# Kernel optimization log

Measured on AMD Instinct MI355X. Metric: run time of the kernel, lower is better.

Reference implementation:

```python
import jax, jax.numpy as jnp
import numpy as np
from jax import lax

B, TZ, TT = 16, 2048, 512
D, DFF, L, V, HEADS = 256, 1024, 6, 512, 4
CH, HID, K, FLOWS, G = 256, 256, 5, 4, 256
PAD_ID = 0
NEG = -1e9
SCALE = 0.02


def setup_inputs():
    key = jax.random.key(0)
    ks = jax.random.split(key, 20)
    n = lambda i, shape, s=SCALE: jax.random.normal(ks[i], shape, jnp.float32) * s
    return {
        'z': jax.random.normal(ks[0], (B, TZ, CH), jnp.float32),
        'text': jax.random.randint(ks[1], (B, TT), 1, V),  # low=1 so no pad tokens
        'cond': jax.random.normal(ks[2], (B, G), jnp.float32),
        'embed': n(3, (V, D), 1.0),
        'wq': n(4, (L, D, D)), 'wk': n(5, (L, D, D)), 'wv': n(6, (L, D, D)), 'wo': n(7, (L, D, D)),
        'bq': jnp.zeros((L, D)), 'bk': jnp.zeros((L, D)), 'bv': jnp.zeros((L, D)), 'bo': jnp.zeros((L, D)),
        'ln1_g': jnp.ones((L, D)), 'ln1_b': jnp.zeros((L, D)),
        'ln2_g': jnp.ones((L, D)), 'ln2_b': jnp.zeros((L, D)),
        'w1': n(8, (L, D, DFF)), 'b1': jnp.zeros((L, DFF)),
        'w2': n(9, (L, DFF, D)), 'b2': jnp.zeros((L, D)),
        'mu_w': n(10, (D, D)), 'mu_b': jnp.zeros((D,)),
        'lv_w': n(11, (D, D)), 'lv_b': jnp.zeros((D,)),
        'flow_in': n(12, (FLOWS, CH // 2, HID)), 'flow_in_b': jnp.zeros((FLOWS, HID)),
        'flow_cond': n(13, (FLOWS, G, HID)),
        'flow_conv': n(14, (FLOWS, K, HID, HID)), 'flow_conv_b': jnp.zeros((FLOWS, HID)),
        'flow_out': n(15, (FLOWS, HID, CH // 2)), 'flow_out_b': jnp.zeros((FLOWS, CH // 2)),
    }


def _pos_encoding(length, d):
    pos = np.arange(length)[:, None].astype(np.float32)
    i = np.arange(d)[None, :]
    angle = pos / np.power(10000.0, (2 * (i // 2)) / d)
    pe = np.where(i % 2 == 0, np.sin(angle), np.cos(angle))
    return jnp.asarray(pe, jnp.float32)


def _ln(x, g, b):
    m = jnp.mean(x, -1, keepdims=True)
    v = jnp.var(x, -1, keepdims=True)
    return g * (x - m) * lax.rsqrt(v + 1e-6) + b


def _mha(x, wq, wk, wv, wo, bq, bk, bv, bo, bias):
    Bq, T, _ = x.shape
    dh = D // HEADS
    heads = lambda y: y.reshape(Bq, T, HEADS, dh).transpose(0, 2, 1, 3)
    q, k, v = heads(x @ wq + bq), heads(x @ wk + bk), heads(x @ wv + bv)
    scores = jnp.einsum('bhqd,bhkd->bhqk', q, k) / jnp.sqrt(jnp.float32(dh)) + bias
    attn = jax.nn.softmax(scores, axis=-1)
    out = jnp.einsum('bhqk,bhkd->bhqd', attn, v).transpose(0, 2, 1, 3).reshape(Bq, T, D)
    return out @ wo + bo


def _mas_path(logp, text_mask):
    # Viterbi monotonic alignment: each latent frame t maps to text index j(t),
    # j nondecreasing with steps in {0, 1}, start at 0, end at last valid token.
    Bq, Tz, Tt = logp.shape
    Q0 = jnp.where(jnp.arange(Tt) == 0, logp[:, 0, :], NEG)

    def fwd(Q, lt):
        Qs = jnp.concatenate([jnp.full((Bq, 1), NEG, Q.dtype), Q[:, :-1]], axis=1)
        return lt + jnp.maximum(Q, Qs), Qs > Q  # choice True => came from j-1

    _, choices = lax.scan(fwd, Q0, jnp.swapaxes(logp, 0, 1)[1:])  # [Tz-1,B,Tt]
    j_last = jnp.sum(text_mask, axis=1).astype(jnp.int32) - 1

    def bwd(j, ch):
        c = jnp.take_along_axis(ch, j[:, None], axis=1)[:, 0]
        jp = j - c.astype(jnp.int32)
        return jp, jp

    _, path_rev = lax.scan(bwd, j_last, choices[::-1])
    path = jnp.concatenate([path_rev[::-1], j_last[None]], axis=0)  # [Tz,B]
    return jnp.swapaxes(path, 0, 1)


def _forward(z, text, cond, embed, wq, wk, wv, wo, bq, bk, bv, bo, ln1_g, ln1_b, ln2_g, ln2_b,
             w1, b1, w2, b2, mu_w, mu_b, lv_w, lv_b,
             flow_in, flow_in_b, flow_cond, flow_conv, flow_conv_b, flow_out, flow_out_b):
    text_mask = text != PAD_ID  # [B,TT]
    bias = jnp.where(text_mask[:, None, None, :], 0.0, NEG)
    # text encoder: scaled embedding + sinusoidal PE + post-LN transformer blocks
    h = embed[text] * jnp.sqrt(jnp.float32(D)) + _pos_encoding(TT, D)[None]
    for l in range(L):
        h = _ln(h + _mha(h, wq[l], wk[l], wv[l], wo[l], bq[l], bk[l], bv[l], bo[l], bias), ln1_g[l], ln1_b[l])
        ffn = jax.nn.relu(h @ w1[l] + b1[l]) @ w2[l] + b2[l]
        h = _ln(h + ffn, ln2_g[l], ln2_b[l])
    mu = h @ mu_w + mu_b
    logvar = h @ lv_w + lv_b
    # residual coupling flows (mean-only, conditioned on global vector)
    zc = z
    for f in range(FLOWS):
        x0, x1 = jnp.split(zc, 2, axis=-1)
        hh = x0 @ flow_in[f] + flow_in_b[f] + (cond @ flow_cond[f])[:, None, :]
        hh = jnp.tanh(lax.conv_general_dilated(hh, flow_conv[f], (1,), 'SAME', rhs_dilation=(1,),
                                               dimension_numbers=('NWC', 'WIO', 'NWC')) + flow_conv_b[f])
        m = hh @ flow_out[f] + flow_out_b[f]
        zc = jnp.concatenate([x1 + m, x0], axis=-1)  # coupling + flip
    # gaussian log-likelihood between latent frames and text distributions
    spr = jnp.exp(-logvar)  # [B,TT,D]
    nc1 = jnp.sum(-0.5 * jnp.log(2.0 * jnp.pi) - 0.5 * logvar, axis=-1)  # [B,TT]
    nc2 = jnp.einsum('btd,bjd->btj', -0.5 * zc * zc, spr)
    nc3 = jnp.einsum('btd,bjd->btj', zc, mu * spr)
    nc4 = jnp.sum(-0.5 * mu * mu * spr, axis=-1)  # [B,TT]
    logp = nc1[:, None, :] + nc2 + nc3 + nc4[:, None, :]  # [B,TZ,TT]
    logp = jnp.where(text_mask[:, None, :], logp, NEG)
    path = _mas_path(logp, text_mask)  # [B,TZ] int32
    ctx = mu[jnp.arange(B)[:, None], path]  # expand text mu along latent time
    return ctx, h


def reference(z, text, cond, embed, wq, wk, wv, wo, bq, bk, bv, bo, ln1_g, ln1_b, ln2_g, ln2_b,
              w1, b1, w2, b2, mu_w, mu_b, lv_w, lv_b,
              flow_in, flow_in_b, flow_cond, flow_conv, flow_conv_b, flow_out, flow_out_b):
    return _forward(z, text, cond, embed, wq, wk, wv, wo, bq, bk, bv, bo, ln1_g, ln1_b, ln2_g, ln2_b,
                    w1, b1, w2, b2, mu_w, mu_b, lv_w, lv_b,
                    flow_in, flow_in_b, flow_cond, flow_conv, flow_conv_b, flow_out, flow_out_b)
```

## Files before the change

kernel.cpp:

```cpp
#include <hip/hip_runtime.h>

#define BB 16
#define TZ_ 2048
#define TT_ 512
#define D_ 256
#define DFF_ 1024
#define L_ 6
#define HEADS_ 4
#define DH_ 64
#define CH_ 256
#define HID_ 256
#define KCV 5
#define FLOWS_ 4
#define G_ 256
#define NEGF (-1000000000.0f)
#define LOG2PI 1.8378770664093453f

typedef unsigned short u16;
typedef __attribute__((ext_vector_type(8))) short short8v;
typedef __attribute__((ext_vector_type(4))) float f32x4;

__device__ __forceinline__ float wsum(float v){
#pragma unroll
  for (int o = 32; o; o >>= 1) v += __shfl_xor(v, o);
  return v;
}
__device__ __forceinline__ u16 f2bf(float x){
  unsigned u = __float_as_uint(x);
  return (u16)((u + 0x7FFFu + ((u >> 16) & 1u)) >> 16);
}
__device__ __forceinline__ float bf2f(u16 h){
  return __uint_as_float(((unsigned)h) << 16);
}
__device__ __forceinline__ unsigned pk2f(float a, float b){
  return __builtin_amdgcn_perm(__float_as_uint(b), __float_as_uint(a), 0x07060302u);
}
__device__ __forceinline__ float trnc(float f){
  return __uint_as_float(__float_as_uint(f) & 0xFFFF0000u);
}
__device__ __forceinline__ void cvt8t(float4 x, float4 y, uint4 &hi, uint4 &lo){
  hi.x = pk2f(x.x, x.y); hi.y = pk2f(x.z, x.w);
  hi.z = pk2f(y.x, y.y); hi.w = pk2f(y.z, y.w);
  float r0 = x.x - trnc(x.x), r1 = x.y - trnc(x.y), r2 = x.z - trnc(x.z), r3 = x.w - trnc(x.w);
  float r4 = y.x - trnc(y.x), r5 = y.y - trnc(y.y), r6 = y.z - trnc(y.z), r7 = y.w - trnc(y.w);
  lo.x = pk2f(r0, r1); lo.y = pk2f(r2, r3); lo.z = pk2f(r4, r5); lo.w = pk2f(r6, r7);
}
__device__ __forceinline__ unsigned rneh(float f){
  unsigned v = __float_as_uint(f);
  return (v + 0x7FFFu + ((v >> 16) & 1u)) & 0xFFFF0000u;
}
__device__ __forceinline__ void cvt8r(float4 x, float4 y, uint4 &hi, uint4 &lo){
  unsigned h0=rneh(x.x), h1=rneh(x.y), h2=rneh(x.z), h3=rneh(x.w);
  unsigned h4=rneh(y.x), h5=rneh(y.y), h6=rneh(y.z), h7=rneh(y.w);
  hi.x = h1 | (h0>>16); hi.y = h3 | (h2>>16); hi.z = h5 | (h4>>16); hi.w = h7 | (h6>>16);
  float r0 = x.x - __uint_as_float(h0), r1 = x.y - __uint_as_float(h1);
  float r2 = x.z - __uint_as_float(h2), r3 = x.w - __uint_as_float(h3);
  float r4 = y.x - __uint_as_float(h4), r5 = y.y - __uint_as_float(h5);
  float r6 = y.z - __uint_as_float(h6), r7 = y.w - __uint_as_float(h7);
  lo.x = pk2f(r0, r1); lo.y = pk2f(r2, r3); lo.z = pk2f(r4, r5); lo.w = pk2f(r6, r7);
}

__global__ void k_pe(float* __restrict__ pe){
  int t = blockIdx.x, d = threadIdx.x;
  double e = (double)(2*(d>>1)) / (double)D_;
  double ang = (double)t * pow(10000.0, -e);
  pe[t*D_ + d] = (float)(((d&1)==0) ? sin(ang) : cos(ang));
}
__global__ void k_embed(const int* __restrict__ text, const float* __restrict__ emb,
                        const float* __restrict__ pe, float* __restrict__ h){
  int row = blockIdx.x, d = threadIdx.x;
  h[(size_t)row*D_ + d] = emb[(size_t)text[row]*D_ + d]*16.0f + pe[(row%TT_)*D_ + d];
}

__global__ __launch_bounds__(256) void k_wt(
  const float* __restrict__ wq, const float* __restrict__ wk,
  const float* __restrict__ wv, const float* __restrict__ wo,
  const float* __restrict__ mu_w, const float* __restrict__ lv_w,
  const float* __restrict__ w1, const float* __restrict__ w2,
  float* __restrict__ QKVT, float* __restrict__ OT, float* __restrict__ MULVT,
  float* __restrict__ W1T, float* __restrict__ W2T)
{
  __shared__ float td[64][65];
  const int s = blockIdx.y, tile = blockIdx.x, t = threadIdx.x;
  const float* inb; float* outb; int istride, ostride;
  if (s < 24){
    int l = s>>2, wsel = s&3;
    const float* w = (wsel==0?wq:wsel==1?wk:wsel==2?wv:wo);
    inb = w + (size_t)l*65536; istride = 256;
    if (wsel < 3) outb = QKVT + (size_t)l*196608 + wsel*65536;
    else          outb = OT   + (size_t)l*65536;
    ostride = 256;
  } else if (s < 26){
    inb = (s==24 ? mu_w : lv_w); istride = 256;
    outb = MULVT + (size_t)(s-24)*65536; ostride = 256;
  } else if (s < 50){
    int idx = s-26, l = idx>>2, b2 = idx&3;
    inb = w1 + (size_t)l*262144 + b2*256; istride = 1024;
    outb = W1T + (size_t)l*262144 + (size_t)b2*65536; ostride = 256;
  } else {
    int idx = s-50, l = idx>>2, b2 = idx&3;
    inb = w2 + (size_t)l*262144 + (size_t)b2*65536; istride = 256;
    outb = W2T + (size_t)l*262144 + b2*256; ostride = 1024;
  }
  const int kt = (tile>>2)*64, nt = (tile&3)*64;
  const int r = t>>2, cq = (t&3)*16;
#pragma unroll
  for (int c=0;c<16;c+=4){
    float4 v = *(const float4*)(inb + (size_t)(kt + r)*istride + nt + cq + c);
    td[r][cq+c+0]=v.x; td[r][cq+c+1]=v.y; td[r][cq+c+2]=v.z; td[r][cq+c+3]=v.w;
  }
  __syncthreads();
#pragma unroll
  for (int c=0;c<16;c+=4){
    float4 v = make_float4(td[cq+c+0][r], td[cq+c+1][r], td[cq+c+2][r], td[cq+c+3][r]);
    *(float4*)(outb + (size_t)(nt + r)*ostride + kt + cq + c) = v;
  }
}

__global__ __launch_bounds__(256) void k_vt(const float* __restrict__ QKV, float* __restrict__ VT){
  __shared__ float td[64][65];
  const int b = blockIdx.z, dt = blockIdx.x, jt = blockIdx.y, t = threadIdx.x;
  const float* inb = QKV + (size_t)b*512*768 + 512;
  float* outb = VT + (size_t)b*131072;
  const int r = t>>2, cq = (t&3)*16;
#pragma unroll
  for (int c=0;c<16;c+=4){
    float4 v = *(const float4*)(inb + (size_t)(jt*64 + r)*768 + dt*64 + cq + c);
    td[r][cq+c+0]=v.x; td[r][cq+c+1]=v.y; td[r][cq+c+2]=v.z; td[r][cq+c+3]=v.w;
  }
  __syncthreads();
#pragma unroll
  for (int c=0;c<16;c+=4){
    float4 v = make_float4(td[cq+c+0][r], td[cq+c+1][r], td[cq+c+2][r], td[cq+c+3][r]);
    *(float4*)(outb + (size_t)(dt*64 + r)*512 + jt*64 + cq + c) = v;
  }
}

__global__ void k_bcat(const float* __restrict__ bq, const float* __restrict__ bk,
                       const float* __restrict__ bv, const float* __restrict__ mu_b,
                       const float* __restrict__ lv_b,
                       float* __restrict__ BQKV, float* __restrict__ MULVB){
  int i = blockIdx.x*256 + threadIdx.x;
  if (i < 4608){
    int l = i/768, c = i%768;
    float v = c<256 ? bq[l*256+c] : (c<512 ? bk[l*256+c-256] : bv[l*256+c-512]);
    BQKV[i] = v;
  } else if (i < 5120){
    int c = i-4608;
    MULVB[c] = c<256 ? mu_b[c] : lv_b[c-256];
  }
}

template<int WN, int EPI, int AM, int BMD>
__global__ __launch_bounds__(256,2) void k_mg(
  const void* __restrict__ Ap, const void* __restrict__ ApL, int lda, int azhi, int azlo,
  const void* __restrict__ Bp, const void* __restrict__ BpL, int ldb, int bzhi, int bzlo,
  const float* __restrict__ bias, const int* __restrict__ text,
  const float* __restrict__ nc1v, const float* __restrict__ nc4v,
  float* __restrict__ C, int ldc, int czhi, int czlo, int K)
{
  constexpr int BN = WN*32;
  __shared__ u16 AH[4096], AL[4096];
  __shared__ u16 BH[BN*32], BL[BN*32];
  char* AHB=(char*)AH; char* ALB=(char*)AL; char* BHB=(char*)BH; char* BLB=(char*)BL;
  const int t = threadIdx.x, z = blockIdx.z;
  const int m0 = blockIdx.y*128, n0 = blockIdx.x*BN;
  const size_t aoff = (size_t)(z>>2)*azhi + (size_t)(z&3)*azlo;
  const size_t boff = (size_t)(z>>2)*bzhi + (size_t)(z&3)*bzlo;
  const size_t coff = (size_t)(z>>2)*czhi + (size_t)(z&3)*czlo;
  const int w = t>>6, l = t&63;
  const int wr = (w>>1)*64, wc = (w&1)*(WN*16);
  const int lr = l&15, lg = l>>4;
  const int srow = t>>1, sseg = t&1;
  const int q  = (srow>>1)&3;
  const int wo0 = srow*64 + ((((sseg<<1)|0)^q)<<4);
  const int wo1 = srow*64 + ((((sseg<<1)|1)^q)<<4);
  const bool bact = (WN==4) || (t < 128);
  const int qa = ((wr+lr)>>1)&3, qb2 = ((wc+lr)>>1)&3;
  const int raBase = (wr+lr)*64 + ((lg^qa)<<4);
  const int rbBase = (wc+lr)*64 + ((lg^qb2)<<4);

  const float* Af = nullptr; const u16* AfH = nullptr; const u16* AfL = nullptr;
  if constexpr (AM==0 || AM==2){ Af = (const float*)Ap + aoff; }
  else { AfH = (const u16*)Ap + aoff; AfL = (const u16*)ApL + aoff; }
  const float* Bf = nullptr; const u16* BfH = nullptr; const u16* BfL = nullptr;
  if constexpr (BMD==0){ Bf = (const float*)Bp + boff; }
  else { BfH = (const u16*)Bp + boff; BfL = (const u16*)BpL + boff; }

  f32x4 acc[4][WN];
#pragma unroll
  for (int i=0;i<4;i++)
#pragma unroll
    for (int j=0;j<WN;j++) acc[i][j] = (f32x4){0.f,0.f,0.f,0.f};

  for (int k0 = 0; k0 < K; k0 += 32){
    uint4 ahi0, ahi1, alo0, alo1;
    if constexpr (AM==0){
      const float* p = Af + (size_t)(m0+srow)*lda + k0 + sseg*16;
      float4 a0=*(const float4*)p, a1=*(const float4*)(p+4);
      float4 a2=*(const float4*)(p+8), a3=*(const float4*)(p+12);
      cvt8t(a0,a1,ahi0,alo0); cvt8t(a2,a3,ahi1,alo1);
    } else if constexpr (AM==1){
      const u16* ph = AfH + (size_t)(m0+srow)*lda + k0 + sseg*16;
      const u16* pl = AfL + (size_t)(m0+srow)*lda + k0 + sseg*16;
      ahi0 = *(const uint4*)ph; ahi1 = *(const uint4*)(ph+8);
      alo0 = *(const uint4*)pl; alo1 = *(const uint4*)(pl+8);
    } else {
      int kg = k0 + sseg*16;
      const float* p = Af + (size_t)(m0+srow)*lda + (kg < 256 ? kg : kg - 256);
      float4 a0=*(const float4*)p, a1=*(const float4*)(p+4);
      float4 a2=*(const float4*)(p+8), a3=*(const float4*)(p+12);
      if (kg >= 256){
        a0.x=-0.5f*a0.x*a0.x; a0.y=-0.5f*a0.y*a0.y; a0.z=-0.5f*a0.z*a0.z; a0.w=-0.5f*a0.w*a0.w;
        a1.x=-0.5f*a1.x*a1.x; a1.y=-0.5f*a1.y*a1.y; a1.z=-0.5f*a1.z*a1.z; a1.w=-0.5f*a1.w*a1.w;
        a2.x=-0.5f*a2.x*a2.x; a2.y=-0.5f*a2.y*a2.y; a2.z=-0.5f*a2.z*a2.z; a2.w=-0.5f*a2.w*a2.w;
        a3.x=-0.5f*a3.x*a3.x; a3.y=-0.5f*a3.y*a3.y; a3.z=-0.5f*a3.z*a3.z; a3.w=-0.5f*a3.w*a3.w;
      }
      cvt8r(a0,a1,ahi0,alo0); cvt8r(a2,a3,ahi1,alo1);
    }
    uint4 bhi0, bhi1, blo0, blo1;
    if (bact){
      if constexpr (BMD==0){
        const float* p = Bf + (size_t)(n0+srow)*ldb + k0 + sseg*16;
        float4 b0=*(const float4*)p, b1=*(const float4*)(p+4);
        float4 b2=*(const float4*)(p+8), b3=*(const float4*)(p+12);
        cvt8t(b0,b1,bhi0,blo0); cvt8t(b2,b3,bhi1,blo1);
      } else {
        const u16* ph = BfH + (size_t)(n0+srow)*ldb + k0 + sseg*16;
        const u16* pl = BfL + (size_t)(n0+srow)*ldb + k0 + sseg*16;
        bhi0 = *(const uint4*)ph; bhi1 = *(const uint4*)(ph+8);
        blo0 = *(const uint4*)pl; blo1 = *(const uint4*)(pl+8);
      }
    }
    __syncthreads();
    *(uint4*)(AHB + wo0) = ahi0;  *(uint4*)(AHB + wo1) = ahi1;
    *(uint4*)(ALB + wo0) = alo0;  *(uint4*)(ALB + wo1) = alo1;
    if (bact){
      *(uint4*)(BHB + wo0) = bhi0;  *(uint4*)(BHB + wo1) = bhi1;
      *(uint4*)(BLB + wo0) = blo0;  *(uint4*)(BLB + wo1) = blo1;
    }
    __syncthreads();
    short8v fah[4], fal[4], fbh[WN], fbl[WN];
#pragma unroll
    for (int i=0;i<4;i++){
      fah[i] = *(short8v*)(AHB + raBase + i*1024);
      fal[i] = *(short8v*)(ALB + raBase + i*1024);
    }
#pragma unroll
    for (int j=0;j<WN;j++){
      fbh[j] = *(short8v*)(BHB + rbBase + j*1024);
      fbl[j] = *(short8v*)(BLB + rbBase + j*1024);
    }
#pragma unroll
    for (int i=0;i<4;i++)
#pragma unroll
      for (int j=0;j<WN;j++){
        acc[i][j] = __builtin_amdgcn_mfma_f32_16x16x32_bf16(fah[i], fbh[j], acc[i][j], 0,0,0);
        acc[i][j] = __builtin_amdgcn_mfma_f32_16x16x32_bf16(fal[i], fbh[j], acc[i][j], 0,0,0);
        acc[i][j] = __builtin_amdgcn_mfma_f32_16x16x32_bf16(fah[i], fbl[j], acc[i][j], 0,0,0);
      }
  }

#pragma unroll
  for (int i=0;i<4;i++){
    int mm0 = m0 + wr + i*16 + (lg<<2);
#pragma unroll
    for (int j=0;j<WN;j++){
      int nn = n0 + wc + j*16 + lr;
      float bs = 0.f; float ncb = 0.f; bool msk = true;
      if (EPI==0 || EPI==1) bs = bias ? bias[nn] : 0.f;
      if (EPI==2) msk = (text[(z>>2)*TT_ + nn] != 0);
      if (EPI==3){ ncb = nc1v[z*TT_+nn] + nc4v[z*TT_+nn]; msk = (text[z*TT_+nn] != 0); }
      f32x4 v = acc[i][j];
#pragma unroll
      for (int r=0;r<4;r++){
        int m = mm0 + r;
        float x;
        if (EPI==0)      x = v[r] + bs;
        else if (EPI==1) x = fmaxf(v[r] + bs, 0.f);
        else if (EPI==2) x = v[r]*0.125f + (msk ? 0.f : NEGF);
        else             x = msk ? (v[r] + ncb) : NEGF;
        C[coff + (size_t)m*ldc + nn] = x;
      }
    }
  }
}

__global__ __launch_bounds__(64) void k_softmax(float* __restrict__ S){
  size_t row = blockIdx.x;
  float* p = S + row*TT_;
  int ln = threadIdx.x;
  float4 a = *(float4*)(p + ln*8);
  float4 b = *(float4*)(p + ln*8 + 4);
  float x[8] = {a.x,a.y,a.z,a.w,b.x,b.y,b.z,b.w};
  float m = x[0];
#pragma unroll
  for (int i=1;i<8;i++) m = fmaxf(m, x[i]);
#pragma unroll
  for (int o2=32;o2;o2>>=1) m = fmaxf(m, __shfl_xor(m, o2));
  float s = 0.f;
#pragma unroll
  for (int i=0;i<8;i++){ x[i] = expf(x[i]-m); s += x[i]; }
  s = wsum(s);
  float inv = 1.0f/s;
  *(float4*)(p + ln*8)     = make_float4(x[0]*inv, x[1]*inv, x[2]*inv, x[3]*inv);
  *(float4*)(p + ln*8 + 4) = make_float4(x[4]*inv, x[5]*inv, x[6]*inv, x[7]*inv);
}

__global__ __launch_bounds__(256) void k_lnres(const float* __restrict__ y,
  const float* __restrict__ g, const float* __restrict__ bb, float* __restrict__ h){
  size_t row = blockIdx.x; int d = threadIdx.x;
  float v = h[row*D_ + d] + y[row*D_ + d];
  float s = wsum(v), s2 = wsum(v*v);
  __shared__ float r1[4], r2[4];
  int w = d >> 6;
  if ((d & 63) == 0){ r1[w] = s; r2[w] = s2; }
  __syncthreads();
  s  = r1[0]+r1[1]+r1[2]+r1[3];
  s2 = r2[0]+r2[1]+r2[2]+r2[3];
  float mean = s * (1.0f/D_);
  float var  = s2 * (1.0f/D_) - mean*mean;
  float inv  = rsqrtf(var + 1e-6f);
  h[row*D_ + d] = g[d]*(v - mean)*inv + bb[d];
}

__global__ __launch_bounds__(256) void k_prep(const float* __restrict__ mulv,
  u16* __restrict__ b2h, u16* __restrict__ b2l,
  float* __restrict__ nc1, float* __restrict__ nc4){
  size_t row = blockIdx.x; int d = threadIdx.x;
  float m = mulv[row*512 + d];
  float lv = mulv[row*512 + 256 + d];
  float sp = expf(-lv);
  float ms = m*sp;
  float s1 = wsum(lv), s2 = wsum(m*ms);
  __shared__ float r1[4], r2[4];
  int w = d >> 6;
  if ((d&63)==0){ r1[w]=s1; r2[w]=s2; }
  __syncthreads();
  if (d == 0){
    nc1[row] = -0.5f*((float)D_*LOG2PI + (r1[0]+r1[1]+r1[2]+r1[3]));
    nc4[row] = -0.5f*(r2[0]+r2[1]+r2[2]+r2[3]);
  }
  unsigned hm = rneh(ms);
  b2h[row*512 + d] = (u16)(hm>>16);
  b2l[row*512 + d] = f2bf(ms - __uint_as_float(hm));
  unsigned hs = rneh(sp);
  b2h[row*512 + 256 + d] = (u16)(hs>>16);
  b2l[row*512 + 256 + d] = f2bf(sp - __uint_as_float(hs));
}

__global__ __launch_bounds__(256) void k_condproj(const float* __restrict__ cond,
  const float* __restrict__ W, float* __restrict__ out){
  const int b = blockIdx.x, n = threadIdx.x;
  float s = 0.f;
  for (int k2=0;k2<G_;k2++) s = fmaf(cond[b*G_ + k2], W[k2*HID_ + n], s);
  out[b*HID_ + n] = s;
}

__global__ void k_wprep2(const float* __restrict__ win, const float* __restrict__ wconv,
                         const float* __restrict__ wout,
                         u16* __restrict__ WITH, u16* __restrict__ WITL,
                         u16* __restrict__ WCTH, u16* __restrict__ WCTL,
                         u16* __restrict__ WOTH, u16* __restrict__ WOTL){
  int i = blockIdx.x*256 + threadIdx.x;
  float wv2; u16 *dh, *dl; int idx;
  if (i < 32768){
    int n = i >> 7, k = i & 127;
    wv2 = win[k*256 + n]; dh = WITH; dl = WITL; idx = i;
  } else if (i < 32768 + 327680){
    int jj = i - 32768;
    int o = jj / 1280, r = jj - o*1280;
    wv2 = wconv[(size_t)r*256 + o]; dh = WCTH; dl = WCTL; idx = jj;
  } else {
    int jj = i - 360448;
    int o = jj >> 8, k = jj & 255;
    wv2 = wout[k*128 + o]; dh = WOTH; dl = WOTL; idx = jj;
  }
  u16 hh = f2bf(wv2);
  dh[idx] = hh;
  dl[idx] = f2bf(wv2 - bf2f(hh));
}

__global__ void k_x0prep2(const float* __restrict__ z, u16* __restrict__ xh, u16* __restrict__ xl){
  size_t i = ((size_t)blockIdx.x*256 + threadIdx.x) << 3;
  size_t m2 = i >> 7; int k = (int)(i & 127);
  const float* src = z + m2*256 + k;
  float4 a = *(const float4*)src; float4 b2 = *(const float4*)(src+4);
  float vv[8] = {a.x,a.y,a.z,a.w,b2.x,b2.y,b2.z,b2.w};
  short8v oh, ol;
#pragma unroll
  for (int r=0;r<8;r++){
    u16 hh = f2bf(vv[r]);
    oh[r] = (short)hh;
    ol[r] = (short)f2bf(vv[r] - bf2f(hh));
  }
  *(short8v*)(xh + i) = oh;
  *(short8v*)(xl + i) = ol;
}

__global__ void k_padzero2(u16* __restrict__ XpH, u16* __restrict__ XpL){
  int i = blockIdx.x*256 + threadIdx.x;
  u16* P = (i >> 14) ? XpL : XpH;
  int ii = i & 16383;
  int b = ii >> 10, rr = (ii >> 8) & 3, c = ii & 255;
  int row = (rr < 2) ? rr : (2048 + rr);
  P[((size_t)b*2052 + row)*256 + c] = 0;
}

template<int EPI, int SPLITOUT>
__global__ __launch_bounds__(256,2) void k_mf2(
  const u16* __restrict__ Ah, const u16* __restrict__ Al, int lda, int padA,
  const u16* __restrict__ Bh, const u16* __restrict__ Bl, int ldb,
  const float* __restrict__ bias, const float* __restrict__ cnd,
  void* __restrict__ CH, void* __restrict__ CL, int ldc, int padC, int K)
{
  __shared__ u16 AsmH[4096], AsmL[4096], BsmH[4096], BsmL[4096];
  char* AHB=(char*)AsmH; char* ALB=(char*)AsmL;
  char* BHB=(char*)BsmH; char* BLB=(char*)BsmL;
  const int t = threadIdx.x;
  const int m0 = blockIdx.y << 7, n0 = blockIdx.x << 7;
  const int w = t >> 6, l = t & 63;
  const int wr = (w >> 1) << 6, wc = (w & 1) << 6;
  const int lr = l & 15, lg = l >> 4;
  const int srow = t >> 1, sseg = t & 1;
  const int q = (srow >> 1) & 3;
  const int wo0 = srow*64 + ((((sseg<<1)|0) ^ q) << 4);
  const int wo1 = srow*64 + ((((sseg<<1)|1) ^ q) << 4);
  const int am = m0 + srow;
  const size_t aoff = (size_t)(am + padA*(am >> 11))*lda + (sseg << 4);
  const u16* AhP = Ah + aoff;
  const u16* AlP = Al + aoff;
  const size_t boff = (size_t)(n0 + srow)*ldb + (sseg << 4);
  const u16* BhP = Bh + boff;
  const u16* BlP = Bl + boff;
  const int qa = ((wr + lr) >> 1) & 3, qb = ((wc + lr) >> 1) & 3;
  const int raBase = (wr + lr)*64 + ((lg ^ qa) << 4);
  const int rbBase = (wc + lr)*64 + ((lg ^ qb) << 4);
  f32x4 acc[4][4];
#pragma unroll
  for (int i=0;i<4;i++)
#pragma unroll
    for (int j=0;j<4;j++) acc[i][j] = (f32x4){0.f,0.f,0.f,0.f};

  for (int k0 = 0; k0 < K; k0 += 32){
    float4 ah0 = *(const float4*)(AhP + k0);
    float4 ah1 = *(const float4*)(AhP + k0 + 8);
    float4 al0 = *(const float4*)(AlP + k0);
    float4 al1 = *(const float4*)(AlP + k0 + 8);
    float4 bh0 = *(const float4*)(BhP + k0);
    float4 bh1 = *(const float4*)(BhP + k0 + 8);
    float4 bl0 = *(const float4*)(BlP + k0);
    float4 bl1 = *(const float4*)(BlP + k0 + 8);
    __syncthreads();
    *(float4*)(AHB + wo0) = ah0;  *(float4*)(AHB + wo1) = ah1;
    *(float4*)(ALB + wo0) = al0;  *(float4*)(ALB + wo1) = al1;
    *(float4*)(BHB + wo0) = bh0;  *(float4*)(BHB + wo1) = bh1;
    *(float4*)(BLB + wo0) = bl0;  *(float4*)(BLB + wo1) = bl1;
    __syncthreads();
    short8v fah[4], fal[4], fbh[4], fbl[4];
#pragma unroll
    for (int i=0;i<4;i++){
      fah[i] = *(short8v*)(AHB + raBase + i*1024);
      fal[i] = *(short8v*)(ALB + raBase + i*1024);
    }
#pragma unroll
    for (int j=0;j<4;j++){
      fbh[j] = *(short8v*)(BHB + rbBase + j*1024);
      fbl[j] = *(short8v*)(BLB + rbBase + j*1024);
    }
#pragma unroll
    for (int i=0;i<4;i++)
#pragma unroll
      for (int j=0;j<4;j++){
        acc[i][j] = __builtin_amdgcn_mfma_f32_16x16x32_bf16(fah[i], fbh[j], acc[i][j], 0, 0, 0);
        acc[i][j] = __builtin_amdgcn_mfma_f32_16x16x32_bf16(fal[i], fbh[j], acc[i][j], 0, 0, 0);
        acc[i][j] = __builtin_amdgcn_mfma_f32_16x16x32_bf16(fah[i], fbl[j], acc[i][j], 0, 0, 0);
      }
  }

#pragma unroll
  for (int i=0;i<4;i++){
    int mbase = m0 + wr + i*16 + (lg << 2);
#pragma unroll
    for (int j=0;j<4;j++){
      int nn = n0 + wc + j*16 + lr;
      float bs = bias[nn];
      f32x4 v = acc[i][j];
#pragma unroll
      for (int r=0;r<4;r++){
        int m = mbase + r;
        float x = v[r] + bs;
        if (EPI == 1) x += cnd[((m >> 11) << 8) + nn];
        if (EPI == 2) x = tanhf(x);
        if (EPI == 3) x += cnd[(size_t)m*256 + 128 + nn];
        size_t ro = (size_t)(m + padC*(m >> 11))*ldc + nn;
        if (SPLITOUT){
          u16 xh = f2bf(x);
          ((u16*)CH)[ro] = xh;
          ((u16*)CL)[ro] = f2bf(x - bf2f(xh));
        } else {
          ((float*)CH)[ro] = x;
        }
      }
    }
  }
}

__global__ void k_x0copy(const float* __restrict__ src, float* __restrict__ dst){
  size_t i = ((size_t)blockIdx.x*256 + threadIdx.x) << 2;
  size_t row = i >> 7; int c = (int)(i & 127);
  *(float4*)(dst + row*256 + 128 + c) = *(const float4*)(src + row*256 + c);
}

#define MCH 8
#define NCHK (TZ_/MCH)
__device__ __forceinline__ void mas_rows(const float* __restrict__ bp, int ch, float* Q,
                                         int ln, unsigned char* __restrict__ cb){
  for (int rr = 0; rr < MCH; rr++){
    int tr = ch*MCH + rr;
    if (tr == 0){
      float q0 = bp[0];
      if (ln == 0) Q[0] = q0;
      continue;
    }
    float4 u0 = *(const float4*)(bp + rr*TT_ + ln*8);
    float4 u1 = *(const float4*)(bp + rr*TT_ + ln*8 + 4);
    float v[8] = {u0.x,u0.y,u0.z,u0.w,u1.x,u1.y,u1.z,u1.w};
    float qp = __shfl_up(Q[7], 1);
    if (ln == 0) qp = NEGF;
    unsigned bits = 0; float qs = qp;
#pragma unroll
    for (int i=0;i<8;i++){
      float old = Q[i];
      if (qs > old) bits |= (1u<<i);
      Q[i] = v[i] + fmaxf(old, qs);
      qs = old;
    }
    cb[(size_t)(tr-1)*64 + ln] = (unsigned char)bits;
  }
}

__global__ __launch_bounds__(512) void k_mas(const float* __restrict__ lp,
  const int* __restrict__ text, unsigned char* __restrict__ cho, int* __restrict__ path)
{
  const int b = blockIdx.x, t = threadIdx.x, ln = t & 63;
  const float* L = lp + (size_t)b*TZ_*TT_;
  __shared__ float buf[3][MCH*TT_];
  __shared__ __align__(16) unsigned char lch[64*64];
  const int frow = t >> 6;
  const int fcol = (t & 63) * 8;
  const size_t gsrc = (size_t)frow*TT_ + fcol;
  unsigned char* cb = cho + (size_t)b*TZ_*64;
  {
    float4 a0 = *(const float4*)(L + gsrc);
    float4 a1 = *(const float4*)(L + gsrc + 4);
    float4 c0 = *(const float4*)(L + (size_t)MCH*TT_ + gsrc);
    float4 c1 = *(const float4*)(L + (size_t)MCH*TT_ + gsrc + 4);
    *(float4*)&buf[0][(size_t)frow*TT_+fcol]   = a0;
    *(float4*)&buf[0][(size_t)frow*TT_+fcol+4] = a1;
    *(float4*)&buf[1][(size_t)frow*TT_+fcol]   = c0;
    *(float4*)&buf[1][(size_t)frow*TT_+fcol+4] = c1;
  }
  float4 pA0 = *(const float4*)(L + (size_t)2*MCH*TT_ + gsrc);
  float4 pA1 = *(const float4*)(L + (size_t)2*MCH*TT_ + gsrc + 4);
  float4 pB0 = *(const float4*)(L + (size_t)3*MCH*TT_ + gsrc);
  float4 pB1 = *(const float4*)(L + (size_t)3*MCH*TT_ + gsrc + 4);
  __syncthreads();
  float Q[8];
#pragma unroll
  for (int i=0;i<8;i++) Q[i] = NEGF;
  int cur = 0;
#define MAS_STEP(CH, P0, P1) do { \
    int wslot = cur + 2; if (wslot >= 3) wslot -= 3; \
    if ((CH) + 2 < NCHK){ \
      *(float4*)&buf[wslot][(size_t)frow*TT_+fcol]   = P0; \
      *(float4*)&buf[wslot][(size_t)frow*TT_+fcol+4] = P1; \
    } \
    if ((CH) + 4 < NCHK){ \
      P0 = *(const float4*)(L + (size_t)((CH)+4)*MCH*TT_ + gsrc); \
      P1 = *(const float4*)(L + (size_t)((CH)+4)*MCH*TT_ + gsrc + 4); \
    } \
    if (t < 64) mas_rows(&buf[cur][0], (CH), Q, ln, cb); \
    __syncthreads(); \
    cur++; if (cur >= 3) cur = 0; \
  } while(0)
  for (int ch = 0; ch < NCHK; ch += 2){
    MAS_STEP(ch,   pA0, pA1);
    MAS_STEP(ch+1, pB0, pB1);
  }
#undef MAS_STEP
  int j = 0;
  if (t < 64){
    int cnt = 0;
#pragma unroll
    for (int i=0;i<8;i++) cnt += (text[b*TT_ + ln*8 + i] != 0) ? 1 : 0;
#pragma unroll
    for (int o2=32;o2;o2>>=1) cnt += __shfl_xor(cnt, o2);
    j = cnt - 1;
  }
  if (t == 0) path[b*TZ_ + TZ_-1] = j;
  __syncthreads();
  for (int tc = TZ_-1; tc >= 1; tc -= 64){
    int ns = min(64, tc);
    if (t < 256){
      int s = t >> 2, c = (t & 3) << 4;
      if (s < ns)
        *(float4*)&lch[s*64 + c] = *(const float4*)&cb[(size_t)(tc-1-s)*64 + c];
    }
    __syncthreads();
    if (t == 0){
      for (int s=0;s<ns;s++){
        unsigned bits = lch[s*64 + (j>>3)];
        j -= (int)((bits >> (j&7)) & 1u);
        path[b*TZ_ + tc - s - 1] = j;
      }
    }
    __syncthreads();
  }
}

__global__ void k_gather(const float* __restrict__ mulv, const int* __restrict__ path,
  const float* __restrict__ h, float* __restrict__ out){
  size_t i = (size_t)blockIdx.x*256 + threadIdx.x;
  const size_t N4 = (size_t)BB*TZ_*(D_/4);
  const size_t H4 = (size_t)BB*TT_*(D_/4);
  if (i < N4){
    size_t row = i >> 6; int c = (int)(i & 63);
    int b = (int)(row >> 11);
    int pj = path[row];
    ((float4*)out)[i] = *(const float4*)(mulv + ((size_t)b*TT_ + pj)*512 + (size_t)c*4);
  } else if (i < N4 + H4){
    size_t k2 = i - N4;
    ((float4*)out)[i] = ((const float4*)h)[k2];
  }
}

extern "C" void kernel_launch(void* const* d_in, const int* in_sizes, int n_in,
                              void* d_out, int out_size, void* d_ws, size_t ws_size,
                              hipStream_t stream)
{
  (void)in_sizes; (void)n_in; (void)out_size; (void)ws_size;
  const float* z      = (const float*)d_in[0];
  const int*   text   = (const int*)  d_in[1];
  const float* cond   = (const float*)d_in[2];
  const float* emb    = (const float*)d_in[3];
  const float* wq     = (const float*)d_in[4];
  const float* wk     = (const float*)d_in[5];
  const float* wv     = (const float*)d_in[6];
  const float* wo     = (const float*)d_in[7];
  const float* bq     = (const float*)d_in[8];
  const float* bk     = (const float*)d_in[9];
  const float* bv     = (const float*)d_in[10];
  const float* bo     = (const float*)d_in[11];
  const float* ln1g   = (const float*)d_in[12];
  const float* ln1b   = (const float*)d_in[13];
  const float* ln2g   = (const float*)d_in[14];
  const float* ln2b   = (const float*)d_in[15];
  const float* w1     = (const float*)d_in[16];
  const float* b1     = (const float*)d_in[17];
  const float* w2     = (const float*)d_in[18];
  const float* b2     = (const float*)d_in[19];
  const float* mu_w   = (const float*)d_in[20];
  const float* mu_b   = (const float*)d_in[21];
  const float* lv_w   = (const float*)d_in[22];
  const float* lv_b   = (const float*)d_in[23];
  const float* f_in   = (const float*)d_in[24];
  const float* f_in_b = (const float*)d_in[25];
  const float* f_cond = (const float*)d_in[26];
  const float* f_conv = (const float*)d_in[27];
  const float* f_convb= (const float*)d_in[28];
  const float* f_out  = (const float*)d_in[29];
  const float* f_outb = (const float*)d_in[30];

  float* ws = (float*)d_ws;
  size_t o = 0;
  float* PE   = ws + o; o += (size_t)131072;
  float* H    = ws + o; o += (size_t)2097152;
  float* MULV = ws + o; o += (size_t)4194304;
  float* NC1  = ws + o; o += (size_t)8192;
  float* NC4  = ws + o; o += (size_t)8192;
  float* CONDP= ws + o; o += (size_t)4096;
  int*   PATH = (int*)(ws + o); o += (size_t)32768;
  u16*  B2H  = (u16*)(ws + o); o += (size_t)2097152;
  u16*  B2L  = (u16*)(ws + o); o += (size_t)2097152;
  float* BIGS = ws + o; o += (size_t)16777216;
  float* BUF1 = ws + o; o += (size_t)4587520;
  float* BUF2 = ws + o; o += (size_t)10485760;
  float* ZCA  = ws + o; o += (size_t)8388608;
  float* ZCB  = ws + o; o += (size_t)8388608;

  float* QKV = BUF2;
  float* Yb  = QKV + 6291456;
  float* VT  = Yb + 2097152;
  float* ATTO= QKV;
  float* QKVT = ZCA;
  float* OT   = QKVT + 1179648;
  float* W1T  = OT + 393216;
  float* W2T  = W1T + 1572864;
  float* MULVT= W2T + 1572864;
  float* BQKV = MULVT + 131072;
  float* MULVB= BQKV + 4608;
  u16*  X0H = (u16*)BUF1;
  u16*  X0L = X0H + 4194304;
  u16*  WITH = X0L + 4194304;
  u16*  WITL = WITH + 32768;
  u16*  WCTH = WITL + 32768;
  u16*  WCTL = WCTH + 327680;
  u16*  WOTH = WCTL + 327680;
  u16*  WOTL = WOTH + 32768;
  u16*  XpH = (u16*)BIGS;
  u16*  XpL = XpH + 8404992;
  u16*  H2H = (u16*)BUF2;
  u16*  H2L = H2H + 8388608;
  unsigned char* CHO = (unsigned char*)ZCA;

  k_pe   <<<dim3(TT_),    dim3(D_), 0, stream>>>(PE);
  k_embed<<<dim3(BB*TT_), dim3(D_), 0, stream>>>(text, emb, PE, H);
  k_wt   <<<dim3(16,74), 256, 0, stream>>>(wq,wk,wv,wo,mu_w,lv_w,w1,w2, QKVT,OT,MULVT,W1T,W2T);
  k_bcat <<<dim3(20), 256, 0, stream>>>(bq,bk,bv,mu_b,lv_b, BQKV, MULVB);

  for (int l=0;l<L_;l++){
    k_mg<4,0,0,0><<<dim3(6,64,1),256,0,stream>>>(
      H, nullptr, 256, 0,0,  QKVT + (size_t)l*196608, nullptr, 256, 0,0,
      BQKV + l*768, nullptr, nullptr, nullptr, QKV, 768, 0,0, 256);
    k_vt <<<dim3(4,8,16),256,0,stream>>>(QKV, VT);
    k_mg<4,2,0,0><<<dim3(4,4,64),256,0,stream>>>(
      QKV, nullptr, 768, 393216, 64,  QKV+256, nullptr, 768, 393216, 64,
      nullptr, text, nullptr, nullptr, BIGS, 512, 1048576, 262144, 64);
    k_softmax<<<dim3(BB*HEADS_*TT_),64,0,stream>>>(BIGS);
    k_mg<2,0,0,0><<<dim3(1,4,64),256,0,stream>>>(
      BIGS, nullptr, 512, 1048576, 262144,  VT, nullptr, 512, 131072, 32768,
      nullptr, nullptr, nullptr, nullptr, Yb, 256, 131072, 64, 512);
    k_mg<4,0,0,0><<<dim3(2,64,1),256,0,stream>>>(
      Yb, nullptr, 256, 0,0,  OT + (size_t)l*65536, nullptr, 256, 0,0,
      bo + l*256, nullptr, nullptr, nullptr, ATTO, 256, 0,0, 256);
    k_lnres<<<dim3(BB*TT_),256,0,stream>>>(ATTO, ln1g+l*D_, ln1b+l*D_, H);
    k_mg<4,1,0,0><<<dim3(8,64,1),256,0,stream>>>(
      H, nullptr, 256, 0,0,  W1T + (size_t)l*262144, nullptr, 256, 0,0,
      b1 + l*1024, nullptr, nullptr, nullptr, BIGS, 1024, 0,0, 256);
    k_mg<4,0,0,0><<<dim3(2,64,1),256,0,stream>>>(
      BIGS, nullptr, 1024, 0,0,  W2T + (size_t)l*262144, nullptr, 1024, 0,0,
      b2 + l*256, nullptr, nullptr, nullptr, ATTO, 256, 0,0, 1024);
    k_lnres<<<dim3(BB*TT_),256,0,stream>>>(ATTO, ln2g+l*D_, ln2b+l*D_, H);
  }

  k_mg<4,0,0,0><<<dim3(4,64,1),256,0,stream>>>(
    H, nullptr, 256, 0,0,  MULVT, nullptr, 256, 0,0,
    MULVB, nullptr, nullptr, nullptr, MULV, 512, 0,0, 256);
  k_prep<<<dim3(BB*TT_),256,0,stream>>>(MULV, B2H, B2L, NC1, NC4);

  k_padzero2<<<dim3(128),256,0,stream>>>(XpH, XpL);
  const float* zsrc = z;
  for (int f=0; f<FLOWS_; f++){
    k_condproj<<<dim3(BB),256,0,stream>>>(cond, f_cond + (size_t)f*G_*HID_, CONDP);
    k_wprep2<<<dim3(1536),256,0,stream>>>(f_in + (size_t)f*(CH_/2)*HID_,
                                          f_conv + (size_t)f*KCV*HID_*HID_,
                                          f_out + (size_t)f*HID_*(CH_/2),
                                          WITH, WITL, WCTH, WCTL, WOTH, WOTL);
    k_x0prep2<<<dim3(2048),256,0,stream>>>(zsrc, X0H, X0L);
    k_mf2<1,1><<<dim3(2,256),256,0,stream>>>(X0H, X0L, 128, 0, WITH, WITL, 128,
        f_in_b + f*HID_, CONDP, (void*)(XpH + 512), (void*)(XpL + 512), 256, 4, 128);
    k_mf2<2,1><<<dim3(2,256),256,0,stream>>>(XpH, XpL, 256, 4, WCTH, WCTL, 1280,
        f_convb + f*HID_, nullptr, (void*)H2H, (void*)H2L, 256, 0, 1280);
    float* zdst = (f & 1) ? ZCB : ZCA;
    k_mf2<3,0><<<dim3(1,256),256,0,stream>>>(H2H, H2L, 256, 0, WOTH, WOTL, 256,
        f_outb + f*(CH_/2), zsrc, (void*)zdst, nullptr, 256, 0, 256);
    k_x0copy<<<dim3(4096),256,0,stream>>>(zsrc, zdst);
    zsrc = zdst;
  }

  k_mg<4,3,2,1><<<dim3(4,16,16),256,0,stream>>>(
    zsrc, nullptr, 256, 2097152, 524288,
    B2H, B2L, 512, 1048576, 262144,
    nullptr, text, NC1, NC4, BIGS, 512, 4194304, 1048576, 512);

  k_mas<<<dim3(BB),512,0,stream>>>(BIGS, text, CHO, PATH);
  k_gather<<<dim3((BB*TZ_*D_/4 + BB*TT_*D_/4)/256),256,0,stream>>>(MULV, PATH, H, (float*)d_out);
}
```

Baseline: 2.483 ms.

## Pipeline MAS forward/backtrack, fuse flow prep kernels, widen softmax blocks

Restructures the MAS kernel. The forward DP gets a swizzled LDS layout and register-prefetched rows, and the backtrack prefetches choice bytes into a triple-buffered LDS ring with per-row lookahead instead of one serial loop per 64-step chunk. The three flow prep kernels (weight transpose/split, x0 split, cond projection) merge into one launch, and the x0 copy is folded into the output GEMM epilogue. Softmax now handles four rows per 256-thread block. This cuts launch overhead and serial latency in MAS at the cost of more register pressure and more complex indexing.

After: 2.685 ms. +8.2%, slower.

```diff
diff --git a/kernel.cpp b/kernel.cpp
--- a/kernel.cpp
+++ b/kernel.cpp
@@ -286,10 +286,10 @@
   }
 }
 
-__global__ __launch_bounds__(64) void k_softmax(float* __restrict__ S){
-  size_t row = blockIdx.x;
+__global__ __launch_bounds__(256) void k_softmax(float* __restrict__ S){
+  size_t row = (size_t)blockIdx.x*4 + (threadIdx.x >> 6);
   float* p = S + row*TT_;
-  int ln = threadIdx.x;
+  int ln = threadIdx.x & 63;
   float4 a = *(float4*)(p + ln*8);
   float4 b = *(float4*)(p + ln*8 + 4);
   float x[8] = {a.x,a.y,a.z,a.w,b.x,b.y,b.z,b.w};
@@ -349,53 +349,54 @@
   b2l[row*512 + 256 + d] = f2bf(sp - __uint_as_float(hs));
 }
 
-__global__ __launch_bounds__(256) void k_condproj(const float* __restrict__ cond,
-  const float* __restrict__ W, float* __restrict__ out){
-  const int b = blockIdx.x, n = threadIdx.x;
-  float s = 0.f;
-  for (int k2=0;k2<G_;k2++) s = fmaf(cond[b*G_ + k2], W[k2*HID_ + n], s);
-  out[b*HID_ + n] = s;
-}
-
-__global__ void k_wprep2(const float* __restrict__ win, const float* __restrict__ wconv,
-                         const float* __restrict__ wout,
-                         u16* __restrict__ WITH, u16* __restrict__ WITL,
-                         u16* __restrict__ WCTH, u16* __restrict__ WCTL,
-                         u16* __restrict__ WOTH, u16* __restrict__ WOTL){
-  int i = blockIdx.x*256 + threadIdx.x;
-  float wv2; u16 *dh, *dl; int idx;
-  if (i < 32768){
-    int n = i >> 7, k = i & 127;
-    wv2 = win[k*256 + n]; dh = WITH; dl = WITL; idx = i;
-  } else if (i < 32768 + 327680){
-    int jj = i - 32768;
-    int o = jj / 1280, r = jj - o*1280;
-    wv2 = wconv[(size_t)r*256 + o]; dh = WCTH; dl = WCTL; idx = jj;
+__global__ __launch_bounds__(256) void k_fprep(
+  const float* __restrict__ win, const float* __restrict__ wconv, const float* __restrict__ wout,
+  u16* __restrict__ WITH, u16* __restrict__ WITL,
+  u16* __restrict__ WCTH, u16* __restrict__ WCTL,
+  u16* __restrict__ WOTH, u16* __restrict__ WOTL,
+  const float* __restrict__ zsrc, u16* __restrict__ xh, u16* __restrict__ xl,
+  const float* __restrict__ cond, const float* __restrict__ fcw, float* __restrict__ condp)
+{
+  const int bid = blockIdx.x, t = threadIdx.x;
+  if (bid < 1536){
+    int i = bid*256 + t;
+    float wv2; u16 *dh, *dl; int idx;
+    if (i < 32768){
+      int n = i >> 7, k = i & 127;
+      wv2 = win[k*256 + n]; dh = WITH; dl = WITL; idx = i;
+    } else if (i < 360448){
+      int jj = i - 32768;
+      int o = jj / 1280, r = jj - o*1280;
+      wv2 = wconv[(size_t)r*256 + o]; dh = WCTH; dl = WCTL; idx = jj;
+    } else {
+      int jj = i - 360448;
+      int o = jj >> 8, k = jj & 255;
+      wv2 = wout[k*128 + o]; dh = WOTH; dl = WOTL; idx = jj;
+    }
+    u16 hh = f2bf(wv2);
+    dh[idx] = hh;
+    dl[idx] = f2bf(wv2 - bf2f(hh));
+  } else if (bid < 3584){
+    size_t i = ((size_t)(bid-1536)*256 + t) << 3;
+    size_t m2 = i >> 7; int k = (int)(i & 127);
+    const float* src = zsrc + m2*256 + k;
+    float4 a = *(const float4*)src; float4 b2 = *(const float4*)(src+4);
+    float vv[8] = {a.x,a.y,a.z,a.w,b2.x,b2.y,b2.z,b2.w};
+    short8v oh, ol;
+#pragma unroll
+    for (int r=0;r<8;r++){
+      u16 hh = f2bf(vv[r]);
+      oh[r] = (short)hh;
+      ol[r] = (short)f2bf(vv[r] - bf2f(hh));
+    }
+    *(short8v*)(xh + i) = oh;
+    *(short8v*)(xl + i) = ol;
   } else {
-    int jj = i - 360448;
-    int o = jj >> 8, k = jj & 255;
-    wv2 = wout[k*128 + o]; dh = WOTH; dl = WOTL; idx = jj;
-  }
-  u16 hh = f2bf(wv2);
-  dh[idx] = hh;
-  dl[idx] = f2bf(wv2 - bf2f(hh));
-}
-
-__global__ void k_x0prep2(const float* __restrict__ z, u16* __restrict__ xh, u16* __restrict__ xl){
-  size_t i = ((size_t)blockIdx.x*256 + threadIdx.x) << 3;
-  size_t m2 = i >> 7; int k = (int)(i & 127);
-  const float* src = z + m2*256 + k;
-  float4 a = *(const float4*)src; float4 b2 = *(const float4*)(src+4);
-  float vv[8] = {a.x,a.y,a.z,a.w,b2.x,b2.y,b2.z,b2.w};
-  short8v oh, ol;
-#pragma unroll
-  for (int r=0;r<8;r++){
-    u16 hh = f2bf(vv[r]);
-    oh[r] = (short)hh;
-    ol[r] = (short)f2bf(vv[r] - bf2f(hh));
-  }
-  *(short8v*)(xh + i) = oh;
-  *(short8v*)(xl + i) = ol;
+    int b = bid - 3584, n = t;
+    float s = 0.f;
+    for (int k2=0;k2<G_;k2++) s = fmaf(cond[b*G_ + k2], fcw[k2*HID_ + n], s);
+    condp[b*HID_ + n] = s;
+  }
 }
 
 __global__ void k_padzero2(u16* __restrict__ XpH, u16* __restrict__ XpL){
@@ -500,44 +501,36 @@
           ((u16*)CL)[ro] = f2bf(x - bf2f(xh));
         } else {
           ((float*)CH)[ro] = x;
+          if (EPI == 3)
+            ((float*)CH)[(size_t)m*ldc + 128 + nn] = cnd[(size_t)m*256 + nn];
         }
       }
     }
   }
 }
 
-__global__ void k_x0copy(const float* __restrict__ src, float* __restrict__ dst){
-  size_t i = ((size_t)blockIdx.x*256 + threadIdx.x) << 2;
-  size_t row = i >> 7; int c = (int)(i & 127);
-  *(float4*)(dst + row*256 + 128 + c) = *(const float4*)(src + row*256 + c);
-}
-
 #define MCH 8
 #define NCHK (TZ_/MCH)
-__device__ __forceinline__ void mas_rows(const float* __restrict__ bp, int ch, float* Q,
-                                         int ln, unsigned char* __restrict__ cb){
-  for (int rr = 0; rr < MCH; rr++){
-    int tr = ch*MCH + rr;
-    if (tr == 0){
-      float q0 = bp[0];
-      if (ln == 0) Q[0] = q0;
-      continue;
-    }
-    float4 u0 = *(const float4*)(bp + rr*TT_ + ln*8);
-    float4 u1 = *(const float4*)(bp + rr*TT_ + ln*8 + 4);
-    float v[8] = {u0.x,u0.y,u0.z,u0.w,u1.x,u1.y,u1.z,u1.w};
-    float qp = __shfl_up(Q[7], 1);
-    if (ln == 0) qp = NEGF;
-    unsigned bits = 0; float qs = qp;
-#pragma unroll
-    for (int i=0;i<8;i++){
-      float old = Q[i];
-      if (qs > old) bits |= (1u<<i);
-      Q[i] = v[i] + fmaxf(old, qs);
-      qs = old;
-    }
-    cb[(size_t)(tr-1)*64 + ln] = (unsigned char)bits;
-  }
+__device__ __forceinline__ int swsl(int s){ return s ^ ((s>>3)&7); }
+
+__device__ __forceinline__ void mas_row(float4 u0, float4 u1, float* Q, int ln, int tr,
+                                        unsigned char* __restrict__ cb){
+  if (tr == 0){
+    if (ln == 0) Q[0] = u0.x;
+    return;
+  }
+  float v[8] = {u0.x,u0.y,u0.z,u0.w,u1.x,u1.y,u1.z,u1.w};
+  float qp = __shfl_up(Q[7], 1);
+  if (ln == 0) qp = NEGF;
+  unsigned bits = 0; float qs = qp;
+#pragma unroll
+  for (int i=0;i<8;i++){
+    float old = Q[i];
+    if (qs > old) bits |= (1u<<i);
+    Q[i] = v[i] + fmaxf(old, qs);
+    qs = old;
+  }
+  cb[(size_t)(tr-1)*64 + ln] = (unsigned char)bits;
 }
 
 __global__ __launch_bounds__(512) void k_mas(const float* __restrict__ lp,
@@ -546,73 +539,167 @@
   const int b = blockIdx.x, t = threadIdx.x, ln = t & 63;
   const float* L = lp + (size_t)b*TZ_*TT_;
   __shared__ float buf[3][MCH*TT_];
-  __shared__ __align__(16) unsigned char lch[64*64];
-  const int frow = t >> 6;
-  const int fcol = (t & 63) * 8;
-  const size_t gsrc = (size_t)frow*TT_ + fcol;
+  __shared__ __align__(16) unsigned char lch[3][4096];
+  const int frow = t >> 6, k64 = t & 63;
+  const size_t gsrc = (size_t)frow*TT_ + k64*8;
+  char* b0p = (char*)&buf[0][0];
+  char* b1p = (char*)&buf[1][0];
+  char* b2p = (char*)&buf[2][0];
+  char* bufb[3] = {b0p, b1p, b2p};
+  const int wroff = frow*2048;
+  const int ws0 = wroff + (swsl(2*k64)<<4);
+  const int ws1 = wroff + (swsl(2*k64+1)<<4);
+  const int rs0 = swsl(2*ln)<<4;
+  const int rs1 = swsl(2*ln+1)<<4;
   unsigned char* cb = cho + (size_t)b*TZ_*64;
+
   {
     float4 a0 = *(const float4*)(L + gsrc);
     float4 a1 = *(const float4*)(L + gsrc + 4);
     float4 c0 = *(const float4*)(L + (size_t)MCH*TT_ + gsrc);
     float4 c1 = *(const float4*)(L + (size_t)MCH*TT_ + gsrc + 4);
-    *(float4*)&buf[0][(size_t)frow*TT_+fcol]   = a0;
-    *(float4*)&buf[0][(size_t)frow*TT_+fcol+4] = a1;
-    *(float4*)&buf[1][(size_t)frow*TT_+fcol]   = c0;
-    *(float4*)&buf[1][(size_t)frow*TT_+fcol+4] = c1;
+    *(float4*)(b0p + ws0) = a0;  *(float4*)(b0p + ws1) = a1;
+    *(float4*)(b1p + ws0) = c0;  *(float4*)(b1p + ws1) = c1;
   }
   float4 pA0 = *(const float4*)(L + (size_t)2*MCH*TT_ + gsrc);
   float4 pA1 = *(const float4*)(L + (size_t)2*MCH*TT_ + gsrc + 4);
   float4 pB0 = *(const float4*)(L + (size_t)3*MCH*TT_ + gsrc);
   float4 pB1 = *(const float4*)(L + (size_t)3*MCH*TT_ + gsrc + 4);
   __syncthreads();
+
   float Q[8];
 #pragma unroll
   for (int i=0;i<8;i++) Q[i] = NEGF;
+  float4 hA0,hA1,hA2,hA3,hA4,hA5,hA6,hA7;
+  float4 hB0,hB1,hB2,hB3,hB4,hB5,hB6,hB7;
+  if (t < 64){
+    hA0 = *(float4*)(b0p + 0*2048 + rs0); hA1 = *(float4*)(b0p + 0*2048 + rs1);
+    hA2 = *(float4*)(b0p + 1*2048 + rs0); hA3 = *(float4*)(b0p + 1*2048 + rs1);
+    hA4 = *(float4*)(b0p + 2*2048 + rs0); hA5 = *(float4*)(b0p + 2*2048 + rs1);
+    hA6 = *(float4*)(b0p + 3*2048 + rs0); hA7 = *(float4*)(b0p + 3*2048 + rs1);
+  }
   int cur = 0;
-#define MAS_STEP(CH, P0, P1) do { \
-    int wslot = cur + 2; if (wslot >= 3) wslot -= 3; \
-    if ((CH) + 2 < NCHK){ \
-      *(float4*)&buf[wslot][(size_t)frow*TT_+fcol]   = P0; \
-      *(float4*)&buf[wslot][(size_t)frow*TT_+fcol+4] = P1; \
-    } \
-    if ((CH) + 4 < NCHK){ \
-      P0 = *(const float4*)(L + (size_t)((CH)+4)*MCH*TT_ + gsrc); \
-      P1 = *(const float4*)(L + (size_t)((CH)+4)*MCH*TT_ + gsrc + 4); \
-    } \
-    if (t < 64) mas_rows(&buf[cur][0], (CH), Q, ln, cb); \
-    __syncthreads(); \
-    cur++; if (cur >= 3) cur = 0; \
-  } while(0)
-  for (int ch = 0; ch < NCHK; ch += 2){
-    MAS_STEP(ch,   pA0, pA1);
-    MAS_STEP(ch+1, pB0, pB1);
-  }
-#undef MAS_STEP
-  int j = 0;
+  for (int ch = 0; ch < NCHK; ch++){
+    if (ch + 2 < NCHK){
+      char* wb = bufb[(cur+2)%3];
+      if (ch & 1){ *(float4*)(wb + ws0) = pB0; *(float4*)(wb + ws1) = pB1; }
+      else       { *(float4*)(wb + ws0) = pA0; *(float4*)(wb + ws1) = pA1; }
+    }
+    if (ch + 4 < NCHK){
+      const float* src = L + (size_t)(ch+4)*MCH*TT_ + gsrc;
+      if (ch & 1){ pB0 = *(const float4*)src; pB1 = *(const float4*)(src+4); }
+      else       { pA0 = *(const float4*)src; pA1 = *(const float4*)(src+4); }
+    }
+    if (t < 64){
+      char* cbuf = bufb[cur];
+      char* nbuf = bufb[(cur+1)%3];
+      hB0 = *(float4*)(cbuf + 4*2048 + rs0); hB1 = *(float4*)(cbuf + 4*2048 + rs1);
+      hB2 = *(float4*)(cbuf + 5*2048 + rs0); hB3 = *(float4*)(cbuf + 5*2048 + rs1);
+      hB4 = *(float4*)(cbuf + 6*2048 + rs0); hB5 = *(float4*)(cbuf + 6*2048 + rs1);
+      hB6 = *(float4*)(cbuf + 7*2048 + rs0); hB7 = *(float4*)(cbuf + 7*2048 + rs1);
+      mas_row(hA0,hA1,Q,ln, ch*MCH+0, cb);
+      mas_row(hA2,hA3,Q,ln, ch*MCH+1, cb);
+      mas_row(hA4,hA5,Q,ln, ch*MCH+2, cb);
+      mas_row(hA6,hA7,Q,ln, ch*MCH+3, cb);
+      hA0 = *(float4*)(nbuf + 0*2048 + rs0); hA1 = *(float4*)(nbuf + 0*2048 + rs1);
+      hA2 = *(float4*)(nbuf + 1*2048 + rs0); hA3 = *(float4*)(nbuf + 1*2048 + rs1);
+      hA4 = *(float4*)(nbuf + 2*2048 + rs0); hA5 = *(float4*)(nbuf + 2*2048 + rs1);
+      hA6 = *(float4*)(nbuf + 3*2048 + rs0); hA7 = *(float4*)(nbuf + 3*2048 + rs1);
+      mas_row(hB0,hB1,Q,ln, ch*MCH+4, cb);
+      mas_row(hB2,hB3,Q,ln, ch*MCH+5, cb);
+      mas_row(hB4,hB5,Q,ln, ch*MCH+6, cb);
+      mas_row(hB6,hB7,Q,ln, ch*MCH+7, cb);
+    }
+    __syncthreads();
+    cur++; if (cur >= 3) cur = 0;
+  }
+
+  int jl = 0;
   if (t < 64){
     int cnt = 0;
 #pragma unroll
     for (int i=0;i<8;i++) cnt += (text[b*TT_ + ln*8 + i] != 0) ? 1 : 0;
 #pragma unroll
     for (int o2=32;o2;o2>>=1) cnt += __shfl_xor(cnt, o2);
-    j = cnt - 1;
-  }
-  if (t == 0) path[b*TZ_ + TZ_-1] = j;
+    jl = cnt - 1;
+  }
+  if (t == 0) path[b*TZ_ + TZ_-1] = jl;
   __syncthreads();
-  for (int tc = TZ_-1; tc >= 1; tc -= 64){
-    int ns = min(64, tc);
-    if (t < 256){
-      int s = t >> 2, c = (t & 3) << 4;
-      if (s < ns)
-        *(float4*)&lch[s*64 + c] = *(const float4*)&cb[(size_t)(tc-1-s)*64 + c];
-    }
-    __syncthreads();
+
+  const int NP = TZ_ - 1;
+  const int NH = 32;
+  uint* lchU0 = (uint*)&lch[0][0];
+  uint* lchU1 = (uint*)&lch[1][0];
+  uint* lchU2 = (uint*)&lch[2][0];
+  uint* lchU[3] = {lchU0, lchU1, lchU2};
+  const uint* cbU = (const uint*)cb;
+  {
+#pragma unroll
+    for (int k=0;k<2;k++){
+      int d = t + k*512;
+      int p = (d >> 4);
+      lchU0[d] = cbU[(size_t)(2046 - p)*16 + (d & 15)];
+      lchU1[d] = cbU[(size_t)(2046 - (64 + p))*16 + (d & 15)];
+    }
+  }
+  uint uA0, uA1, uB0, uB1;
+  {
+    int d0 = t, d1 = t + 512;
+    uA0 = cbU[(size_t)(2046 - (128 + (d0>>4)))*16 + (d0 & 15)];
+    uA1 = cbU[(size_t)(2046 - (128 + (d1>>4)))*16 + (d1 & 15)];
+    uB0 = cbU[(size_t)(2046 - (192 + (d0>>4)))*16 + (d0 & 15)];
+    uB1 = cbU[(size_t)(2046 - (192 + (d1>>4)))*16 + (d1 & 15)];
+  }
+  __syncthreads();
+
+  int j = jl;
+  unsigned rb0[8], rb1[8]; int rc[8];
+  if (t == 0){
+#pragma unroll
+    for (int qd=0; qd<8; qd++){
+      int cHi = jl >> 3;
+      int cLo = (cHi > 0) ? cHi - 1 : 0;
+      rb1[qd] = lch[0][(qd)*64 + cHi];
+      rb0[qd] = lch[0][(qd)*64 + cLo];
+      rc[qd]  = cHi;
+    }
+  }
+  for (int H = 0; H < NH; H++){
+    if (H + 2 < NH){
+      uint* wb = lchU[(H+2)%3];
+      if (H & 1){ wb[t] = uB0; wb[t+512] = uB1; }
+      else      { wb[t] = uA0; wb[t+512] = uA1; }
+    }
+    if (H + 4 < NH){
+      int d0 = t, d1 = t + 512;
+      int base = (H+4)*64;
+      int p0 = base + (d0>>4), p1 = base + (d1>>4);
+      uint v0 = (p0 <= 2046) ? cbU[(size_t)(2046 - p0)*16 + (d0 & 15)] : 0u;
+      uint v1 = (p1 <= 2046) ? cbU[(size_t)(2046 - p1)*16 + (d1 & 15)] : 0u;
+      if (H & 1){ uB0 = v0; uB1 = v1; }
+      else      { uA0 = v0; uA1 = v1; }
+    }
     if (t == 0){
-      for (int s=0;s<ns;s++){
-        unsigned bits = lch[s*64 + (j>>3)];
-        j -= (int)((bits >> (j&7)) & 1u);
-        path[b*TZ_ + tc - s - 1] = j;
+      int pbase = H*64;
+#pragma unroll 8
+      for (int s = 0; s < 64; s++){
+        int p = pbase + s;
+        if (p < NP){
+          int r = s & 7;
+          int jb = j >> 3;
+          unsigned byte = (jb == rc[r]) ? rb1[r] : rb0[r];
+          j -= (int)((byte >> (j & 7)) & 1u);
+          path[b*TZ_ + 2046 - p] = j;
+          int pn = p + 8;
+          if (pn < NP){
+            int hn = (pn >> 6) % 3, sn = pn & 63;
+            int cHi = j >> 3;
+            int cLo = (cHi > 0) ? cHi - 1 : 0;
+            rb1[r] = lch[hn][sn*64 + cHi];
+            rb0[r] = lch[hn][sn*64 + cLo];
+            rc[r]  = cHi;
+          }
+        }
       }
     }
     __syncthreads();
@@ -727,7 +814,7 @@
     k_mg<4,2,0,0><<<dim3(4,4,64),256,0,stream>>>(
       QKV, nullptr, 768, 393216, 64,  QKV+256, nullptr, 768, 393216, 64,
       nullptr, text, nullptr, nullptr, BIGS, 512, 1048576, 262144, 64);
-    k_softmax<<<dim3(BB*HEADS_*TT_),64,0,stream>>>(BIGS);
+    k_softmax<<<dim3(BB*HEADS_*TT_/4),256,0,stream>>>(BIGS);
     k_mg<2,0,0,0><<<dim3(1,4,64),256,0,stream>>>(
       BIGS, nullptr, 512, 1048576, 262144,  VT, nullptr, 512, 131072, 32768,
       nullptr, nullptr, nullptr, nullptr, Yb, 256, 131072, 64, 512);
@@ -752,12 +839,12 @@
   k_padzero2<<<dim3(128),256,0,stream>>>(XpH, XpL);
   const float* zsrc = z;
   for (int f=0; f<FLOWS_; f++){
-    k_condproj<<<dim3(BB),256,0,stream>>>(cond, f_cond + (size_t)f*G_*HID_, CONDP);
-    k_wprep2<<<dim3(1536),256,0,stream>>>(f_in + (size_t)f*(CH_/2)*HID_,
-                                          f_conv + (size_t)f*KCV*HID_*HID_,
-                                          f_out + (size_t)f*HID_*(CH_/2),
-                                          WITH, WITL, WCTH, WCTL, WOTH, WOTL);
-    k_x0prep2<<<dim3(2048),256,0,stream>>>(zsrc, X0H, X0L);
+    k_fprep<<<dim3(3600),256,0,stream>>>(
+        f_in + (size_t)f*(CH_/2)*HID_, f_conv + (size_t)f*KCV*HID_*HID_,
+        f_out + (size_t)f*HID_*(CH_/2),
+        WITH, WITL, WCTH, WCTL, WOTH, WOTL,
+        zsrc, X0H, X0L,
+        cond, f_cond + (size_t)f*G_*HID_, CONDP);
     k_mf2<1,1><<<dim3(2,256),256,0,stream>>>(X0H, X0L, 128, 0, WITH, WITL, 128,
         f_in_b + f*HID_, CONDP, (void*)(XpH + 512), (void*)(XpL + 512), 256, 4, 128);
     k_mf2<2,1><<<dim3(2,256),256,0,stream>>>(XpH, XpL, 256, 4, WCTH, WCTL, 1280,
@@ -765,7 +852,6 @@
     float* zdst = (f & 1) ? ZCB : ZCA;
     k_mf2<3,0><<<dim3(1,256),256,0,stream>>>(H2H, H2L, 256, 0, WOTH, WOTL, 256,
         f_outb + f*(CH_/2), zsrc, (void*)zdst, nullptr, 256, 0, 256);
-    k_x0copy<<<dim3(4096),256,0,stream>>>(zsrc, zdst);
     zsrc = zdst;
   }
 
```
